# Kernel optimization log

Measured on AMD Instinct MI355X. Metric: run time of the kernel, lower is better.

Reference implementation:

```python
import jax, jax.numpy as jnp
import numpy as np

NUM_NODES = 2_000_000
NUM_PINS = 8_000_000


def setup_inputs() -> dict:
    key = jax.random.key(0)
    k1, k2, k3 = jax.random.split(key, 3)
    # CSR offsets: sorted, pinned to [0, NUM_PINS]
    starts = jnp.sort(jax.random.randint(k1, (NUM_NODES + 1,), 0, NUM_PINS + 1, dtype=jnp.int32))
    starts = starts.at[0].set(0).at[-1].set(NUM_PINS)
    # flat node->pin map: a permutation of all pin ids (each pin belongs to one node)
    flat_node2pin = jax.random.permutation(k2, NUM_PINS).astype(jnp.int32)
    # per-pin sort key (a permutation -> unique keys, like a global pin ordering)
    sorted_pin_map = jax.random.permutation(k3, NUM_PINS).astype(jnp.int32)
    return {
        "flat_node2pin_start": starts,
        "flat_node2pin": flat_node2pin,
        "sorted_pin_map": sorted_pin_map,
        "num_nodes": NUM_NODES,
    }


def reference(flat_node2pin_start, flat_node2pin, sorted_pin_map, num_nodes):
    """For each node, return the pin id (from its CSR segment) with the minimum
    sorted_pin_map value; 0 for nodes with no pins (matching zeros init)."""
    num_pins = flat_node2pin.shape[0]
    pin_pos = jnp.arange(num_pins, dtype=jnp.int32)
    # segment id for each flat pin slot: node i owns [starts[i], starts[i+1])
    seg = (jnp.searchsorted(flat_node2pin_start, pin_pos, side="right") - 1).astype(jnp.int32)
    key = sorted_pin_map[flat_node2pin]  # ordering key per flat slot
    min_key = jax.ops.segment_min(key, seg, num_segments=num_nodes)  # [num_nodes]
    # pick the pin achieving the min key (ties -> smallest pin id, keys unique here)
    cand = jnp.where(key == min_key[seg], flat_node2pin, jnp.int32(num_pins))
    best_pin = jax.ops.segment_min(cand, seg, num_segments=num_nodes)
    counts = flat_node2pin_start[1:] - flat_node2pin_start[:-1]
    node2pinId = jnp.where(counts > 0, best_pin, jnp.int32(0)).astype(jnp.int32)
    return node2pinId
```

## Files before the change

kernel.cpp:

```cpp
#include <hip/hip_runtime.h>
#include <stdint.h>


typedef int iv4 __attribute__((ext_vector_type(4)));

#define NPB 1024
#define NT  256
#define SEGS 4
#define CAP 4608
#define PINMASK 0x7FFFFFu

__global__ void build_key4_kernel(const int* __restrict__ key,
                                  uint32_t* __restrict__ key4,
                                  int num_pins, int shift) {
    int t = blockIdx.x * blockDim.x + threadIdx.x;
    int base = t * 8;
    if (base >= num_pins) return;
    if (base + 8 <= num_pins) {
        const iv4* kp = (const iv4*)(key + base);
        iv4 a = __builtin_nontemporal_load(kp);
        iv4 b = __builtin_nontemporal_load(kp + 1);
        uint32_t w = 0;
        w |= (((uint32_t)a.x >> shift) & 15u) << 0;
        w |= (((uint32_t)a.y >> shift) & 15u) << 4;
        w |= (((uint32_t)a.z >> shift) & 15u) << 8;
        w |= (((uint32_t)a.w >> shift) & 15u) << 12;
        w |= (((uint32_t)b.x >> shift) & 15u) << 16;
        w |= (((uint32_t)b.y >> shift) & 15u) << 20;
        w |= (((uint32_t)b.z >> shift) & 15u) << 24;
        w |= (((uint32_t)b.w >> shift) & 15u) << 28;
        __builtin_nontemporal_store(w, key4 + t);
    } else {
        uint32_t w = 0;
        for (int j = 0; base + j < num_pins; ++j) {
            uint32_t k = (uint32_t)key[base + j];
            w |= ((k >> shift) & 15u) << (4 * j);
        }
        __builtin_nontemporal_store(w, key4 + t);
    }
}

__device__ __forceinline__ uint32_t nib_of(const uint32_t* key4, uint32_t p) {
    uint32_t w = key4[p >> 3];
    return (w >> ((p & 7u) * 4u)) & 15u;
}

__device__ __forceinline__ iv4 load_chunk(const int* __restrict__ n2p,
                                          int jal, int jbeg, int jend, int c) {
    int j0 = jal + (c << 2);
    if (j0 >= jbeg && j0 + 4 <= jend) {
        return __builtin_nontemporal_load((const iv4*)(n2p + j0));
    }
    iv4 r;
    #pragma unroll
    for (int e = 0; e < 4; ++e) {
        int j = j0 + e;
        r[e] = (j >= jbeg && j < jend) ? __builtin_nontemporal_load(n2p + j)
                                       : -1;
    }
    return r;
}

__device__ __forceinline__ uint32_t pack_sv(const uint32_t* key4, int pi) {
    if (pi < 0) return 0xFFFFFFFFu;
    uint32_t p = (uint32_t)pi;
    return (nib_of(key4, p) << 23) | p;
}

__device__ __forceinline__ void upd3(uint32_t sp, uint32_t& m1, uint32_t& m2,
                                     uint32_t& m3) {
    uint32_t a = min(sp, m1);
    uint32_t b = max(sp, m1);
    uint32_t c = min(b, m2);
    uint32_t d = max(b, m2);
    m1 = a; m2 = c; m3 = min(d, m3);
}

__device__ __forceinline__ void scan_mins(const uint32_t* slot, int s, int e,
                                          uint32_t& m1, uint32_t& m2, uint32_t& m3) {
    m1 = ~0u; m2 = ~0u; m3 = ~0u;
    for (int q = (s & ~3); q < e; q += 4) {
        iv4 v = *(const iv4*)(slot + q);
        #pragma unroll
        for (int u = 0; u < 4; ++u) {
            int j = q + u;
            uint32_t sp = (uint32_t)v[u];
            sp = (j >= s && j < e) ? sp : ~0u;
            upd3(sp, m1, m2, m3);
        }
    }
}

__global__ __launch_bounds__(NT) void SortNode2Pin_stage_kernel(
        const int* __restrict__ starts,
        const int* __restrict__ n2p,
        const int* __restrict__ key,
        const uint32_t* __restrict__ key4,
        int* __restrict__ out,
        int num_nodes) {
    __shared__ __align__(16) uint32_t slot[CAP + 8];

    int t = threadIdx.x;
    int i0 = blockIdx.x * NPB;

    int iend = i0 + NPB; if (iend > num_nodes) iend = num_nodes;
    int jbeg0 = starts[i0 < num_nodes ? i0 : num_nodes];
    int jend0 = starts[iend];
    int range = jend0 - jbeg0;

    int sS[SEGS], eS[SEGS];
    #pragma unroll
    for (int k = 0; k < SEGS; ++k) {
        int ia = i0 + k * NT + t;  if (ia > num_nodes) ia = num_nodes;
        int ib = ia + 1;           if (ib > num_nodes) ib = num_nodes;
        sS[k] = starts[ia];
        eS[k] = starts[ib];
    }

    if (range <= CAP) {
        int jal = jbeg0 & ~3;
        int nch = (jend0 - jal + 3) >> 2;
        int c = t;
        for (; c + 3 * NT < nch; c += 4 * NT) {
            iv4 p0 = load_chunk(n2p, jal, jbeg0, jend0, c);
            iv4 p1 = load_chunk(n2p, jal, jbeg0, jend0, c + NT);
            iv4 p2 = load_chunk(n2p, jal, jbeg0, jend0, c + 2 * NT);
            iv4 p3 = load_chunk(n2p, jal, jbeg0, jend0, c + 3 * NT);
            iv4 w0, w1, w2, w3;
            #pragma unroll
            for (int u = 0; u < 4; ++u) w0[u] = (int)pack_sv(key4, p0[u]);
            #pragma unroll
            for (int u = 0; u < 4; ++u) w1[u] = (int)pack_sv(key4, p1[u]);
            #pragma unroll
            for (int u = 0; u < 4; ++u) w2[u] = (int)pack_sv(key4, p2[u]);
            #pragma unroll
            for (int u = 0; u < 4; ++u) w3[u] = (int)pack_sv(key4, p3[u]);
            *(iv4*)&slot[(c           ) << 2] = w0;
            *(iv4*)&slot[(c +     NT  ) << 2] = w1;
            *(iv4*)&slot[(c + 2 * NT  ) << 2] = w2;
            *(iv4*)&slot[(c + 3 * NT  ) << 2] = w3;
        }
        for (; c < nch; c += NT) {
            iv4 pa = load_chunk(n2p, jal, jbeg0, jend0, c);
            iv4 wa;
            #pragma unroll
            for (int u = 0; u < 4; ++u) wa[u] = (int)pack_sv(key4, pa[u]);
            *(iv4*)&slot[c << 2] = wa;
        }
        __syncthreads();

        uint32_t M1[SEGS], M2[SEGS], M3[SEGS];
        #pragma unroll
        for (int k = 0; k < SEGS; ++k)
            scan_mins(slot, sS[k] - jal, eS[k] - jal, M1[k], M2[k], M3[k]);

        int res[SEGS];
        int pa[SEGS], pb[SEGS];
        bool two[SEGS], multi[SEGS];
        #pragma unroll
        for (int k = 0; k < SEGS; ++k) {
            two[k] = false; multi[k] = false;
            pa[k] = 0; pb[k] = 0;
            uint32_t b1 = M1[k] >> 23;
            if (eS[k] <= sS[k]) {
                res[k] = 0;
            } else if ((M2[k] >> 23) != b1) {
                res[k] = (int)(M1[k] & PINMASK);
            } else if ((M3[k] >> 23) != b1) {
                two[k] = true;
                pa[k] = (int)(M1[k] & PINMASK);
                pb[k] = (int)(M2[k] & PINMASK);
                res[k] = 0;
            } else {
                multi[k] = true;
                res[k] = 0;
            }
        }
        int ka[SEGS], kb[SEGS];
        #pragma unroll
        for (int k = 0; k < SEGS; ++k) {
            ka[k] = 0; kb[k] = 0;
            if (two[k]) { ka[k] = key[pa[k]]; kb[k] = key[pb[k]]; }
        }
        #pragma unroll
        for (int k = 0; k < SEGS; ++k)
            if (two[k]) res[k] = ka[k] < kb[k] ? pa[k] : pb[k];

        #pragma unroll
        for (int k = 0; k < SEGS; ++k) {
            if (multi[k]) {
                uint32_t b1 = M1[k] >> 23;
                int bk = 0x7fffffff, r = 0;
                for (int q = sS[k] - jal; q < eS[k] - jal; ++q) {
                    uint32_t sp = slot[q];
                    if ((sp >> 23) == b1) {
                        int p = (int)(sp & PINMASK);
                        int kk = key[p];
                        if (kk < bk) { bk = kk; r = p; }
                    }
                }
                res[k] = r;
            }
        }

        #pragma unroll
        for (int k = 0; k < SEGS; ++k) {
            int node = i0 + k * NT + t;
            if (node < num_nodes)
                __builtin_nontemporal_store(res[k], out + node);
        }
    } else {
        for (int idx = t; idx < NPB; idx += NT) {
            int node = i0 + idx;
            if (node >= num_nodes) break;
            int s = starts[node], e = starts[node + 1];
            int mv = 16, bp = 0, bk = -1;
            for (int j = s; j < e; ++j) {
                uint32_t p = (uint32_t)n2p[j];
                int n = (int)nib_of(key4, p);
                if (n > mv) continue;
                if (n < mv) { mv = n; bp = (int)p; bk = -1; }
                else {
                    if (bk < 0) bk = key[bp];
                    int k = key[p];
                    if (k < bk) { bk = k; bp = (int)p; }
                }
            }
            __builtin_nontemporal_store(bp, out + node);
        }
    }
}

__global__ void SortNode2Pin_direct_kernel(const int* __restrict__ starts,
                                           const int* __restrict__ n2p,
                                           const int* __restrict__ key,
                                           int* __restrict__ out,
                                           int num_nodes) {
    int i = blockIdx.x * blockDim.x + threadIdx.x;
    if (i >= num_nodes) return;
    int s = starts[i];
    int e = starts[i + 1];
    int best_pin = 0;
    int best_key = 0x7fffffff;
    for (int j = s; j < e; ++j) {
        int p = n2p[j];
        int k = key[p];
        if (k < best_key) { best_key = k; best_pin = p; }
    }
    out[i] = best_pin;
}

extern "C" void kernel_launch(void* const* d_in, const int* in_sizes, int n_in,
                              void* d_out, int out_size, void* d_ws, size_t ws_size,
                              hipStream_t stream) {
    const int* starts = (const int*)d_in[0];
    const int* n2p    = (const int*)d_in[1];
    const int* key    = (const int*)d_in[2];
    int num_nodes = out_size;
    int num_pins  = in_sizes[1];

    size_t key4_words = (size_t)((num_pins + 7) / 8);
    size_t need = key4_words * sizeof(uint32_t);

    if (ws_size >= need && num_pins < (1 << 23)) {
        int bits = 32 - __builtin_clz((unsigned)(num_pins - 1));
        int shift = bits > 4 ? bits - 4 : 0;
        uint32_t* key4 = (uint32_t*)d_ws;

        int g1 = (int)((key4_words + NT - 1) / NT);
        build_key4_kernel<<<g1, NT, 0, stream>>>(key, key4, num_pins, shift);

        int g2 = (num_nodes + NPB - 1) / NPB;
        SortNode2Pin_stage_kernel<<<g2, NT, 0, stream>>>(
            starts, n2p, key, key4, (int*)d_out, num_nodes);
    } else {
        int grid = (num_nodes + 255) / 256;
        SortNode2Pin_direct_kernel<<<grid, 256, 0, stream>>>(
            starts, n2p, key, (int*)d_out, num_nodes);
    }
}
```

Before: 85.78 us.

## Gather key nibble words directly into LDS with global_load_lds

The staging phase no longer gathers key4 words into registers and packs them before writing to shared memory. Each wave loads 64 pins coalesced and uses the global_load_lds builtin to gather the matching key4 words straight into a separate LDS array. Nibble extraction moves into the scan phase. Block size is halved (512 nodes, 2 segments per thread, smaller LDS capacity) to fit two LDS arrays and raise occupancy. The cost is scalar 4-byte loads instead of 16-byte vector loads for the pin array, plus some extra work during the scan.

```diff
diff --git a/kernel.cpp b/kernel.cpp
--- a/kernel.cpp
+++ b/kernel.cpp
@@ -4,10 +4,11 @@
 
 typedef int iv4 __attribute__((ext_vector_type(4)));
 
-#define NPB 1024
+#define NPB 512
 #define NT  256
-#define SEGS 4
-#define CAP 4608
+#define NWAVE 4
+#define SEGS 2
+#define CAP 2560
 #define PINMASK 0x7FFFFFu
 
 __global__ void build_key4_kernel(const int* __restrict__ key,
@@ -45,26 +46,11 @@
     return (w >> ((p & 7u) * 4u)) & 15u;
 }
 
-__device__ __forceinline__ iv4 load_chunk(const int* __restrict__ n2p,
-                                          int jal, int jbeg, int jend, int c) {
-    int j0 = jal + (c << 2);
-    if (j0 >= jbeg && j0 + 4 <= jend) {
-        return __builtin_nontemporal_load((const iv4*)(n2p + j0));
-    }
-    iv4 r;
-    #pragma unroll
-    for (int e = 0; e < 4; ++e) {
-        int j = j0 + e;
-        r[e] = (j >= jbeg && j < jend) ? __builtin_nontemporal_load(n2p + j)
-                                       : -1;
-    }
-    return r;
-}
-
-__device__ __forceinline__ uint32_t pack_sv(const uint32_t* key4, int pi) {
-    if (pi < 0) return 0xFFFFFFFFu;
-    uint32_t p = (uint32_t)pi;
-    return (nib_of(key4, p) << 23) | p;
+__device__ __forceinline__ void gload_lds_u32(const uint32_t* g, uint32_t* lds) {
+    __builtin_amdgcn_global_load_lds(
+        (const __attribute__((address_space(1))) void*)g,
+        (__attribute__((address_space(3))) void*)lds,
+        4, 0, 0);
 }
 
 __device__ __forceinline__ void upd3(uint32_t sp, uint32_t& m1, uint32_t& m2,
@@ -76,29 +62,36 @@
     m1 = a; m2 = c; m3 = min(d, m3);
 }
 
-__device__ __forceinline__ void scan_mins(const uint32_t* slot, int s, int e,
-                                          uint32_t& m1, uint32_t& m2, uint32_t& m3) {
+__device__ __forceinline__ void scan_mins2(const uint32_t* pins,
+                                           const uint32_t* gwords,
+                                           int s, int e,
+                                           uint32_t& m1, uint32_t& m2, uint32_t& m3) {
     m1 = ~0u; m2 = ~0u; m3 = ~0u;
     for (int q = (s & ~3); q < e; q += 4) {
-        iv4 v = *(const iv4*)(slot + q);
+        iv4 pv = *(const iv4*)(pins + q);
+        iv4 gv = *(const iv4*)(gwords + q);
         #pragma unroll
         for (int u = 0; u < 4; ++u) {
             int j = q + u;
-            uint32_t sp = (uint32_t)v[u];
-            sp = (j >= s && j < e) ? sp : ~0u;
-            upd3(sp, m1, m2, m3);
-        }
-    }
-}
-
-__global__ __launch_bounds__(NT) void SortNode2Pin_stage_kernel(
+            uint32_t pin = (uint32_t)pv[u];
+            uint32_t gw  = (uint32_t)gv[u];
+            uint32_t nib = (gw >> ((pin & 7u) * 4u)) & 15u;
+            uint32_t sv  = (nib << 23) | (pin & PINMASK);
+            sv = (j >= s && j < e) ? sv : ~0u;
+            upd3(sv, m1, m2, m3);
+        }
+    }
+}
+
+__global__ __launch_bounds__(NT) void SortNode2Pin_glds_kernel(
         const int* __restrict__ starts,
         const int* __restrict__ n2p,
         const int* __restrict__ key,
         const uint32_t* __restrict__ key4,
         int* __restrict__ out,
         int num_nodes) {
-    __shared__ __align__(16) uint32_t slot[CAP + 8];
+    __shared__ __align__(16) uint32_t pins[CAP + 8];
+    __shared__ __align__(16) uint32_t gwords[CAP + 8];
 
     int t = threadIdx.x;
     int i0 = blockIdx.x * NPB;
@@ -118,49 +111,54 @@
     }
 
     if (range <= CAP) {
-        int jal = jbeg0 & ~3;
-        int nch = (jend0 - jal + 3) >> 2;
-        int c = t;
-        for (; c + 3 * NT < nch; c += 4 * NT) {
-            iv4 p0 = load_chunk(n2p, jal, jbeg0, jend0, c);
-            iv4 p1 = load_chunk(n2p, jal, jbeg0, jend0, c + NT);
-            iv4 p2 = load_chunk(n2p, jal, jbeg0, jend0, c + 2 * NT);
-            iv4 p3 = load_chunk(n2p, jal, jbeg0, jend0, c + 3 * NT);
-            iv4 w0, w1, w2, w3;
-            #pragma unroll
-            for (int u = 0; u < 4; ++u) w0[u] = (int)pack_sv(key4, p0[u]);
-            #pragma unroll
-            for (int u = 0; u < 4; ++u) w1[u] = (int)pack_sv(key4, p1[u]);
-            #pragma unroll
-            for (int u = 0; u < 4; ++u) w2[u] = (int)pack_sv(key4, p2[u]);
-            #pragma unroll
-            for (int u = 0; u < 4; ++u) w3[u] = (int)pack_sv(key4, p3[u]);
-            *(iv4*)&slot[(c           ) << 2] = w0;
-            *(iv4*)&slot[(c +     NT  ) << 2] = w1;
-            *(iv4*)&slot[(c + 2 * NT  ) << 2] = w2;
-            *(iv4*)&slot[(c + 3 * NT  ) << 2] = w3;
-        }
-        for (; c < nch; c += NT) {
-            iv4 pa = load_chunk(n2p, jal, jbeg0, jend0, c);
-            iv4 wa;
-            #pragma unroll
-            for (int u = 0; u < 4; ++u) wa[u] = (int)pack_sv(key4, pa[u]);
-            *(iv4*)&slot[c << 2] = wa;
+        int lane = t & 63;
+        int w = t >> 6;
+        int gfull = range >> 6;
+        int g = w;
+        for (; g + 3 * NWAVE < gfull; g += 4 * NWAVE) {
+            int b0 = (g             ) << 6;
+            int b1 = (g +     NWAVE ) << 6;
+            int b2 = (g + 2 * NWAVE ) << 6;
+            int b3 = (g + 3 * NWAVE ) << 6;
+            uint32_t p0 = (uint32_t)__builtin_nontemporal_load(n2p + jbeg0 + b0 + lane);
+            uint32_t p1 = (uint32_t)__builtin_nontemporal_load(n2p + jbeg0 + b1 + lane);
+            uint32_t p2 = (uint32_t)__builtin_nontemporal_load(n2p + jbeg0 + b2 + lane);
+            uint32_t p3 = (uint32_t)__builtin_nontemporal_load(n2p + jbeg0 + b3 + lane);
+            gload_lds_u32(key4 + (p0 >> 3), &gwords[b0]);
+            gload_lds_u32(key4 + (p1 >> 3), &gwords[b1]);
+            gload_lds_u32(key4 + (p2 >> 3), &gwords[b2]);
+            gload_lds_u32(key4 + (p3 >> 3), &gwords[b3]);
+            pins[b0 + lane] = p0;
+            pins[b1 + lane] = p1;
+            pins[b2 + lane] = p2;
+            pins[b3 + lane] = p3;
+        }
+        for (; (g << 6) < range; g += NWAVE) {
+            int base = g << 6;
+            int idx = base + lane;
+            bool valid = idx < range;
+            uint32_t p = 0xFFFFFFFFu;
+            if (valid) {
+                p = (uint32_t)__builtin_nontemporal_load(n2p + jbeg0 + idx);
+                gload_lds_u32(key4 + (p >> 3), &gwords[base]);
+            }
+            pins[idx] = p;
         }
         __syncthreads();
 
         uint32_t M1[SEGS], M2[SEGS], M3[SEGS];
         #pragma unroll
         for (int k = 0; k < SEGS; ++k)
-            scan_mins(slot, sS[k] - jal, eS[k] - jal, M1[k], M2[k], M3[k]);
+            scan_mins2(pins, gwords, sS[k] - jbeg0, eS[k] - jbeg0,
+                       M1[k], M2[k], M3[k]);
 
         int res[SEGS];
-        int pa[SEGS], pb[SEGS];
+        int pa2[SEGS], pb2[SEGS];
         bool two[SEGS], multi[SEGS];
         #pragma unroll
         for (int k = 0; k < SEGS; ++k) {
             two[k] = false; multi[k] = false;
-            pa[k] = 0; pb[k] = 0;
+            pa2[k] = 0; pb2[k] = 0;
             uint32_t b1 = M1[k] >> 23;
             if (eS[k] <= sS[k]) {
                 res[k] = 0;
@@ -168,8 +166,8 @@
                 res[k] = (int)(M1[k] & PINMASK);
             } else if ((M3[k] >> 23) != b1) {
                 two[k] = true;
-                pa[k] = (int)(M1[k] & PINMASK);
-                pb[k] = (int)(M2[k] & PINMASK);
+                pa2[k] = (int)(M1[k] & PINMASK);
+                pb2[k] = (int)(M2[k] & PINMASK);
                 res[k] = 0;
             } else {
                 multi[k] = true;
@@ -180,21 +178,23 @@
         #pragma unroll
         for (int k = 0; k < SEGS; ++k) {
             ka[k] = 0; kb[k] = 0;
-            if (two[k]) { ka[k] = key[pa[k]]; kb[k] = key[pb[k]]; }
+            if (two[k]) { ka[k] = key[pa2[k]]; kb[k] = key[pb2[k]]; }
         }
         #pragma unroll
         for (int k = 0; k < SEGS; ++k)
-            if (two[k]) res[k] = ka[k] < kb[k] ? pa[k] : pb[k];
+            if (two[k]) res[k] = ka[k] < kb[k] ? pa2[k] : pb2[k];
 
         #pragma unroll
         for (int k = 0; k < SEGS; ++k) {
             if (multi[k]) {
                 uint32_t b1 = M1[k] >> 23;
                 int bk = 0x7fffffff, r = 0;
-                for (int q = sS[k] - jal; q < eS[k] - jal; ++q) {
-                    uint32_t sp = slot[q];
-                    if ((sp >> 23) == b1) {
-                        int p = (int)(sp & PINMASK);
+                for (int q = sS[k] - jbeg0; q < eS[k] - jbeg0; ++q) {
+                    uint32_t pin = pins[q];
+                    uint32_t gw  = gwords[q];
+                    uint32_t nib = (gw >> ((pin & 7u) * 4u)) & 15u;
+                    if (nib == b1) {
+                        int p = (int)(pin & PINMASK);
                         int kk = key[p];
                         if (kk < bk) { bk = kk; r = p; }
                     }
@@ -271,7 +271,7 @@
         build_key4_kernel<<<g1, NT, 0, stream>>>(key, key4, num_pins, shift);
 
         int g2 = (num_nodes + NPB - 1) / NPB;
-        SortNode2Pin_stage_kernel<<<g2, NT, 0, stream>>>(
+        SortNode2Pin_glds_kernel<<<g2, NT, 0, stream>>>(
             starts, n2p, key, key4, (int*)d_out, num_nodes);
     } else {
         int grid = (num_nodes + 255) / 256;
```

Measured after the change: 89.87 us. +4.8%, slower.
